# Optimization experiments

Measured on AMD Instinct MI355X. Metric: run time of the kernel, lower is better.

The kernel has to match this reference:

```python
import jax, jax.numpy as jnp
import numpy as np

DISCOUNT_FACTOR = 0.99
AVERAGE_LAMBDA = 0.9
EPS = 1e-8
B, S = 8192, 2048


def setup_inputs() -> dict:
    key = jax.random.key(0)
    k1, k2, k3 = jax.random.split(key, 3)
    values = jax.random.normal(k1, (B, S + 1, 1), jnp.float32)
    rewards = jax.random.normal(k2, (B, S, 1), jnp.float32)
    # binary done flags stored as float, as in the torch module's math
    dones = (jax.random.uniform(k3, (B, S, 1)) < 0.02).astype(jnp.float32)
    # parameter init identical to GammaLambdaLearner.__init__ (atanh of targets)
    raw_gamma = jnp.arctanh(jnp.full((1,), DISCOUNT_FACTOR, jnp.float32))
    raw_lambd = jnp.arctanh(jnp.full((S,), AVERAGE_LAMBDA, jnp.float32))
    return {"values": values, "rewards": rewards, "dones": dones,
            "raw_gamma": raw_gamma, "raw_lambd": raw_lambd}


def reference(values, rewards, dones, raw_gamma, raw_lambd):
    # gamma / lambd properties: tanh then clamp_min(1e-8)
    gamma = jnp.maximum(jnp.tanh(raw_gamma), EPS)          # [1]
    lambd = jnp.maximum(jnp.tanh(raw_lambd), EPS)          # [S]

    # time-major views for the scan: [S, B, 1]
    r = jnp.swapaxes(rewards, 0, 1)
    d = jnp.swapaxes(dones, 0, 1)
    v_next = jnp.swapaxes(values[:, 1:], 0, 1)

    def step(carry, xs):
        # carry: lambda_return[t+1], shape [B, 1]
        r_t, d_t, vn_t, lam_t = xs
        ret = r_t + gamma * (1.0 - d_t) * ((1.0 - lam_t) * vn_t + lam_t * carry)
        return ret, ret

    # backward-in-time recurrence bootstrapped from the final value estimate
    _, outs = jax.lax.scan(step, values[:, -1], (r, d, v_next, lambd), reverse=True)
    return jnp.swapaxes(outs, 0, 1)  # [B, S, 1]
```

## Files before the change

### kernel.cpp

```cpp
#include <hip/hip_runtime.h>
#include <math.h>


#define EPSV 1e-8f

typedef float f32x4 __attribute__((ext_vector_type(4)));

__global__ void precompute_lambda_kernel(const float* __restrict__ raw_gamma,
                                         const float* __restrict__ raw_lambd,
                                         float* __restrict__ lam, int S) {
    int t = blockIdx.x * blockDim.x + threadIdx.x;
    if (t < S) lam[t] = fmaxf(tanhf(raw_lambd[t]), EPSV);
    if (t == S) lam[S] = fmaxf(tanhf(raw_gamma[0]), EPSV);
}

__global__ __launch_bounds__(256) void lamret_kernel(
    const float* __restrict__ values,
    const float* __restrict__ rewards,
    const float* __restrict__ dones,
    const float* __restrict__ raw_gamma,
    const float* __restrict__ raw_lambd,
    const float* __restrict__ lam_pre,
    float* __restrict__ out,
    int S, long vtotal)
{
    constexpr int C = 8;
    __shared__ float aggA[4], aggB[4];

    const int row  = blockIdx.x;
    const int tid  = threadIdx.x;
    const int lane = tid & 63;
    const int wave = tid >> 6;
    const int nwaves = 4;
    const int t0 = tid * C;

    const float* __restrict__ rrow = rewards + (size_t)row * S;
    const float* __restrict__ drow = dones   + (size_t)row * S;
    const float* __restrict__ vrow = values  + (size_t)row * (S + 1);

    const float vlast = vrow[S];

    float gamma;
    if (lam_pre) gamma = lam_pre[S];
    else         gamma = fmaxf(tanhf(raw_gamma[0]), EPSV);

    float a[C], b[C];
    const bool full = (t0 + C <= S) && ((S & 3) == 0);
    if (full) {
        const f32x4* r4 = reinterpret_cast<const f32x4*>(rrow + t0);
        const f32x4* d4 = reinterpret_cast<const f32x4*>(drow + t0);
        f32x4 r01 = r4[0];
        f32x4 r23 = r4[1];
        f32x4 d01 = d4[0];
        f32x4 d23 = d4[1];

        const float* vp = vrow + t0 + 1;
        const int ofs = (int)(((uintptr_t)vp >> 2) & 3);
        const float* base = vp - ofs;
        float vv[C];
        if (ofs == 0) {
            f32x4 w0 = *reinterpret_cast<const f32x4*>(base);
            f32x4 w1 = *reinterpret_cast<const f32x4*>(base + 4);
            #pragma unroll
            for (int i = 0; i < 4; ++i) { vv[i] = w0[i]; vv[4+i] = w1[i]; }
        } else if (base + 12 <= values + vtotal) {
            f32x4 w0 = *reinterpret_cast<const f32x4*>(base);
            f32x4 w1 = *reinterpret_cast<const f32x4*>(base + 4);
            f32x4 w2 = *reinterpret_cast<const f32x4*>(base + 8);
            if (ofs == 1) {
                vv[0]=w0[1]; vv[1]=w0[2]; vv[2]=w0[3];
                vv[3]=w1[0]; vv[4]=w1[1]; vv[5]=w1[2]; vv[6]=w1[3];
                vv[7]=w2[0];
            } else if (ofs == 2) {
                vv[0]=w0[2]; vv[1]=w0[3];
                vv[2]=w1[0]; vv[3]=w1[1]; vv[4]=w1[2]; vv[5]=w1[3];
                vv[6]=w2[0]; vv[7]=w2[1];
            } else {
                vv[0]=w0[3];
                vv[1]=w1[0]; vv[2]=w1[1]; vv[3]=w1[2]; vv[4]=w1[3];
                vv[5]=w2[0]; vv[6]=w2[1]; vv[7]=w2[2];
            }
        } else {
            #pragma unroll
            for (int i = 0; i < C; ++i) vv[i] = vp[i];
        }

        float lm[C];
        if (lam_pre) {
            const f32x4* l4 = reinterpret_cast<const f32x4*>(lam_pre + t0);
            f32x4 l01 = l4[0], l23 = l4[1];
            #pragma unroll
            for (int i = 0; i < 4; ++i) { lm[i] = l01[i]; lm[4+i] = l23[i]; }
        } else {
            #pragma unroll
            for (int i = 0; i < C; ++i) lm[i] = fmaxf(tanhf(raw_lambd[t0 + i]), EPSV);
        }

        float rr[C], dd[C];
        #pragma unroll
        for (int i = 0; i < 4; ++i) { rr[i] = r01[i]; rr[4+i] = r23[i]; }
        #pragma unroll
        for (int i = 0; i < 4; ++i) { dd[i] = d01[i]; dd[4+i] = d23[i]; }

        #pragma unroll
        for (int i = 0; i < C; ++i) {
            float g1d = gamma * (1.0f - dd[i]);
            a[i] = g1d * lm[i];
            b[i] = fmaf(g1d * (1.0f - lm[i]), vv[i], rr[i]);
        }
    } else {
        #pragma unroll
        for (int i = 0; i < C; ++i) {
            int t = t0 + i;
            if (t < S) {
                float lmv = lam_pre ? lam_pre[t] : fmaxf(tanhf(raw_lambd[t]), EPSV);
                float g1d = gamma * (1.0f - drow[t]);
                a[i] = g1d * lmv;
                b[i] = fmaf(g1d * (1.0f - lmv), vrow[t + 1], rrow[t]);
            } else { a[i] = 1.0f; b[i] = 0.0f; }
        }
    }

    float A = 1.0f, Bc = 0.0f;
    #pragma unroll
    for (int i = C - 1; i >= 0; --i) {
        Bc = fmaf(a[i], Bc, b[i]);
        A  = a[i] * A;
    }

    float Ai = A, Bi = Bc;
    #pragma unroll
    for (int off = 1; off < 64; off <<= 1) {
        float Ao = __shfl_down(Ai, off);
        float Bo = __shfl_down(Bi, off);
        if (lane + off < 64) {
            Bi = fmaf(Ai, Bo, Bi);
            Ai = Ai * Ao;
        }
    }
    float Ae = __shfl_down(Ai, 1);
    float Be = __shfl_down(Bi, 1);
    if (lane == 63) { Ae = 1.0f; Be = 0.0f; }

    if (lane == 0) { aggA[wave] = Ai; aggB[wave] = Bi; }
    __syncthreads();
    float TA = 1.0f, TB = 0.0f;
    for (int w2 = wave + 1; w2 < nwaves; ++w2) {
        TB = fmaf(TA, aggB[w2], TB);
        TA = TA * aggA[w2];
    }
    float Af = Ae * TA;
    float Bf = fmaf(Ae, TB, Be);

    float x = fmaf(Af, vlast, Bf);

    float o[C];
    #pragma unroll
    for (int i = C - 1; i >= 0; --i) {
        x = fmaf(a[i], x, b[i]);
        o[i] = x;
    }

    float* __restrict__ orow = out + (size_t)row * S;
    if (full) {
        f32x4* o4 = reinterpret_cast<f32x4*>(orow + t0);
        f32x4 o01, o23;
        #pragma unroll
        for (int i = 0; i < 4; ++i) { o01[i] = o[i]; o23[i] = o[4+i]; }
        __builtin_nontemporal_store(o01, o4);
        __builtin_nontemporal_store(o23, o4 + 1);
    } else {
        for (int i = 0; i < C; ++i)
            if (t0 + i < S) orow[t0 + i] = o[i];
    }
}

extern "C" void kernel_launch(void* const* d_in, const int* in_sizes, int n_in,
                              void* d_out, int out_size, void* d_ws, size_t ws_size,
                              hipStream_t stream) {
    const float* values    = (const float*)d_in[0];
    const float* rewards   = (const float*)d_in[1];
    const float* dones     = (const float*)d_in[2];
    const float* raw_gamma = (const float*)d_in[3];
    const float* raw_lambd = (const float*)d_in[4];
    float* out = (float*)d_out;

    const int S = in_sizes[4];
    const int B = in_sizes[1] / S;
    const long vtotal = in_sizes[0];

    float* lam_pre = nullptr;
    if (ws_size >= (size_t)(S + 1) * sizeof(float)) {
        lam_pre = (float*)d_ws;
        int nthr = 256;
        int nblk = (S + 1 + nthr - 1) / nthr;
        precompute_lambda_kernel<<<nblk, nthr, 0, stream>>>(raw_gamma, raw_lambd, lam_pre, S);
    }

    lamret_kernel<<<B, 256, 0, stream>>>(values, rewards, dones,
                                         raw_gamma, raw_lambd, lam_pre, out, S, vtotal);
}
```

Baseline: 224.0 us.

## Process two rows per block and use nontemporal loads for streamed inputs

```diff
diff --git a/kernel.cpp b/kernel.cpp
--- a/kernel.cpp
+++ b/kernel.cpp
@@ -12,6 +12,100 @@
     int t = blockIdx.x * blockDim.x + threadIdx.x;
     if (t < S) lam[t] = fmaxf(tanhf(raw_lambd[t]), EPSV);
     if (t == S) lam[S] = fmaxf(tanhf(raw_gamma[0]), EPSV);
+}
+
+__device__ __forceinline__ void load_vwindow(const float* __restrict__ vp,
+                                             const float* __restrict__ values,
+                                             long vtotal, float vv[8]) {
+    const int ofs = (int)(((uintptr_t)vp >> 2) & 3);
+    const float* base = vp - ofs;
+    if (ofs == 0) {
+        f32x4 w0 = *reinterpret_cast<const f32x4*>(base);
+        f32x4 w1 = *reinterpret_cast<const f32x4*>(base + 4);
+        #pragma unroll
+        for (int i = 0; i < 4; ++i) { vv[i] = w0[i]; vv[4+i] = w1[i]; }
+    } else if (base + 12 <= values + vtotal) {
+        f32x4 w0 = *reinterpret_cast<const f32x4*>(base);
+        f32x4 w1 = *reinterpret_cast<const f32x4*>(base + 4);
+        f32x4 w2 = *reinterpret_cast<const f32x4*>(base + 8);
+        if (ofs == 1) {
+            vv[0]=w0[1]; vv[1]=w0[2]; vv[2]=w0[3];
+            vv[3]=w1[0]; vv[4]=w1[1]; vv[5]=w1[2]; vv[6]=w1[3];
+            vv[7]=w2[0];
+        } else if (ofs == 2) {
+            vv[0]=w0[2]; vv[1]=w0[3];
+            vv[2]=w1[0]; vv[3]=w1[1]; vv[4]=w1[2]; vv[5]=w1[3];
+            vv[6]=w2[0]; vv[7]=w2[1];
+        } else {
+            vv[0]=w0[3];
+            vv[1]=w1[0]; vv[2]=w1[1]; vv[3]=w1[2]; vv[4]=w1[3];
+            vv[5]=w2[0]; vv[6]=w2[1]; vv[7]=w2[2];
+        }
+    } else {
+        #pragma unroll
+        for (int i = 0; i < 8; ++i) vv[i] = vp[i];
+    }
+}
+
+__device__ __forceinline__ void scan_apply_store(
+    const float a[8], const float b[8], float vlast,
+    float* aggAs, float* aggBs, int lane, int wave,
+    float* __restrict__ orow, int t0, int S, bool full)
+{
+    constexpr int C = 8;
+    const int nwaves = 4;
+
+    float A = 1.0f, Bc = 0.0f;
+    #pragma unroll
+    for (int i = C - 1; i >= 0; --i) {
+        Bc = fmaf(a[i], Bc, b[i]);
+        A  = a[i] * A;
+    }
+
+    float Ai = A, Bi = Bc;
+    #pragma unroll
+    for (int off = 1; off < 64; off <<= 1) {
+        float Ao = __shfl_down(Ai, off);
+        float Bo = __shfl_down(Bi, off);
+        if (lane + off < 64) {
+            Bi = fmaf(Ai, Bo, Bi);
+            Ai = Ai * Ao;
+        }
+    }
+    float Ae = __shfl_down(Ai, 1);
+    float Be = __shfl_down(Bi, 1);
+    if (lane == 63) { Ae = 1.0f; Be = 0.0f; }
+
+    if (lane == 0) { aggAs[wave] = Ai; aggBs[wave] = Bi; }
+    __syncthreads();
+    float TA = 1.0f, TB = 0.0f;
+    for (int w2 = wave + 1; w2 < nwaves; ++w2) {
+        TB = fmaf(TA, aggBs[w2], TB);
+        TA = TA * aggAs[w2];
+    }
+    float Af = Ae * TA;
+    float Bf = fmaf(Ae, TB, Be);
+
+    float x = fmaf(Af, vlast, Bf);
+
+    float o[C];
+    #pragma unroll
+    for (int i = C - 1; i >= 0; --i) {
+        x = fmaf(a[i], x, b[i]);
+        o[i] = x;
+    }
+
+    if (full) {
+        f32x4* o4 = reinterpret_cast<f32x4*>(orow + t0);
+        f32x4 o01, o23;
+        #pragma unroll
+        for (int i = 0; i < 4; ++i) { o01[i] = o[i]; o23[i] = o[4+i]; }
+        __builtin_nontemporal_store(o01, o4);
+        __builtin_nontemporal_store(o23, o4 + 1);
+    } else {
+        for (int i = 0; i < C; ++i)
+            if (t0 + i < S) orow[t0 + i] = o[i];
+    }
 }
 
 __global__ __launch_bounds__(256) void lamret_kernel(
@@ -22,67 +116,60 @@
     const float* __restrict__ raw_lambd,
     const float* __restrict__ lam_pre,
     float* __restrict__ out,
-    int S, long vtotal)
+    int S, long vtotal, int B)
 {
     constexpr int C = 8;
-    __shared__ float aggA[4], aggB[4];
-
-    const int row  = blockIdx.x;
+    __shared__ float aggA[2][4], aggB[2][4];
+
     const int tid  = threadIdx.x;
     const int lane = tid & 63;
     const int wave = tid >> 6;
-    const int nwaves = 4;
-    const int t0 = tid * C;
-
-    const float* __restrict__ rrow = rewards + (size_t)row * S;
-    const float* __restrict__ drow = dones   + (size_t)row * S;
-    const float* __restrict__ vrow = values  + (size_t)row * (S + 1);
-
-    const float vlast = vrow[S];
+    const int t0   = tid * C;
+
+    const int row0 = blockIdx.x * 2;
+    const int row1 = row0 + 1;
+    const bool has1 = (row1 < B);
+
+    const float* __restrict__ rrow0 = rewards + (size_t)row0 * S;
+    const float* __restrict__ drow0 = dones   + (size_t)row0 * S;
+    const float* __restrict__ vrow0 = values  + (size_t)row0 * (S + 1);
+    const float* __restrict__ rrow1 = rewards + (size_t)row1 * S;
+    const float* __restrict__ drow1 = dones   + (size_t)row1 * S;
+    const float* __restrict__ vrow1 = values  + (size_t)row1 * (S + 1);
 
     float gamma;
     if (lam_pre) gamma = lam_pre[S];
     else         gamma = fmaxf(tanhf(raw_gamma[0]), EPSV);
 
-    float a[C], b[C];
+    const float vlast0 = vrow0[S];
+    const float vlast1 = has1 ? vrow1[S] : 0.0f;
+
     const bool full = (t0 + C <= S) && ((S & 3) == 0);
+
+    float a0[C], b0[C], a1[C], b1[C];
     if (full) {
-        const f32x4* r4 = reinterpret_cast<const f32x4*>(rrow + t0);
-        const f32x4* d4 = reinterpret_cast<const f32x4*>(drow + t0);
-        f32x4 r01 = r4[0];
-        f32x4 r23 = r4[1];
-        f32x4 d01 = d4[0];
-        f32x4 d23 = d4[1];
-
-        const float* vp = vrow + t0 + 1;
-        const int ofs = (int)(((uintptr_t)vp >> 2) & 3);
-        const float* base = vp - ofs;
-        float vv[C];
-        if (ofs == 0) {
-            f32x4 w0 = *reinterpret_cast<const f32x4*>(base);
-            f32x4 w1 = *reinterpret_cast<const f32x4*>(base + 4);
-            #pragma unroll
-            for (int i = 0; i < 4; ++i) { vv[i] = w0[i]; vv[4+i] = w1[i]; }
-        } else if (base + 12 <= values + vtotal) {
-            f32x4 w0 = *reinterpret_cast<const f32x4*>(base);
-            f32x4 w1 = *reinterpret_cast<const f32x4*>(base + 4);
-            f32x4 w2 = *reinterpret_cast<const f32x4*>(base + 8);
-            if (ofs == 1) {
-                vv[0]=w0[1]; vv[1]=w0[2]; vv[2]=w0[3];
-                vv[3]=w1[0]; vv[4]=w1[1]; vv[5]=w1[2]; vv[6]=w1[3];
-                vv[7]=w2[0];
-            } else if (ofs == 2) {
-                vv[0]=w0[2]; vv[1]=w0[3];
-                vv[2]=w1[0]; vv[3]=w1[1]; vv[4]=w1[2]; vv[5]=w1[3];
-                vv[6]=w2[0]; vv[7]=w2[1];
-            } else {
-                vv[0]=w0[3];
-                vv[1]=w1[0]; vv[2]=w1[1]; vv[3]=w1[2]; vv[4]=w1[3];
-                vv[5]=w2[0]; vv[6]=w2[1]; vv[7]=w2[2];
-            }
-        } else {
-            #pragma unroll
-            for (int i = 0; i < C; ++i) vv[i] = vp[i];
+        const f32x4* r4_0 = reinterpret_cast<const f32x4*>(rrow0 + t0);
+        const f32x4* d4_0 = reinterpret_cast<const f32x4*>(drow0 + t0);
+        f32x4 r01_0 = __builtin_nontemporal_load(r4_0);
+        f32x4 r23_0 = __builtin_nontemporal_load(r4_0 + 1);
+        f32x4 d01_0 = __builtin_nontemporal_load(d4_0);
+        f32x4 d23_0 = __builtin_nontemporal_load(d4_0 + 1);
+        float vv0[C];
+        load_vwindow(vrow0 + t0 + 1, values, vtotal, vv0);
+
+        f32x4 r01_1 = {0,0,0,0}, r23_1 = {0,0,0,0};
+        f32x4 d01_1 = {0,0,0,0}, d23_1 = {0,0,0,0};
+        float vv1[C];
+        #pragma unroll
+        for (int i = 0; i < C; ++i) vv1[i] = 0.0f;
+        if (has1) {
+            const f32x4* r4_1 = reinterpret_cast<const f32x4*>(rrow1 + t0);
+            const f32x4* d4_1 = reinterpret_cast<const f32x4*>(drow1 + t0);
+            r01_1 = __builtin_nontemporal_load(r4_1);
+            r23_1 = __builtin_nontemporal_load(r4_1 + 1);
+            d01_1 = __builtin_nontemporal_load(d4_1);
+            d23_1 = __builtin_nontemporal_load(d4_1 + 1);
+            load_vwindow(vrow1 + t0 + 1, values, vtotal, vv1);
         }
 
         float lm[C];
@@ -98,15 +185,24 @@
 
         float rr[C], dd[C];
         #pragma unroll
-        for (int i = 0; i < 4; ++i) { rr[i] = r01[i]; rr[4+i] = r23[i]; }
-        #pragma unroll
-        for (int i = 0; i < 4; ++i) { dd[i] = d01[i]; dd[4+i] = d23[i]; }
-
+        for (int i = 0; i < 4; ++i) { rr[i] = r01_0[i]; rr[4+i] = r23_0[i]; }
+        #pragma unroll
+        for (int i = 0; i < 4; ++i) { dd[i] = d01_0[i]; dd[4+i] = d23_0[i]; }
         #pragma unroll
         for (int i = 0; i < C; ++i) {
             float g1d = gamma * (1.0f - dd[i]);
-            a[i] = g1d * lm[i];
-            b[i] = fmaf(g1d * (1.0f - lm[i]), vv[i], rr[i]);
+            a0[i] = g1d * lm[i];
+            b0[i] = fmaf(g1d * (1.0f - lm[i]), vv0[i], rr[i]);
+        }
+        #pragma unroll
+        for (int i = 0; i < 4; ++i) { rr[i] = r01_1[i]; rr[4+i] = r23_1[i]; }
+        #pragma unroll
+        for (int i = 0; i < 4; ++i) { dd[i] = d01_1[i]; dd[4+i] = d23_1[i]; }
+        #pragma unroll
+        for (int i = 0; i < C; ++i) {
+            float g1d = gamma * (1.0f - dd[i]);
+            a1[i] = g1d * lm[i];
+            b1[i] = fmaf(g1d * (1.0f - lm[i]), vv1[i], rr[i]);
         }
     } else {
         #pragma unroll
@@ -114,64 +210,24 @@
             int t = t0 + i;
             if (t < S) {
                 float lmv = lam_pre ? lam_pre[t] : fmaxf(tanhf(raw_lambd[t]), EPSV);
-                float g1d = gamma * (1.0f - drow[t]);
-                a[i] = g1d * lmv;
-                b[i] = fmaf(g1d * (1.0f - lmv), vrow[t + 1], rrow[t]);
-            } else { a[i] = 1.0f; b[i] = 0.0f; }
-        }
-    }
-
-    float A = 1.0f, Bc = 0.0f;
-    #pragma unroll
-    for (int i = C - 1; i >= 0; --i) {
-        Bc = fmaf(a[i], Bc, b[i]);
-        A  = a[i] * A;
-    }
-
-    float Ai = A, Bi = Bc;
-    #pragma unroll
-    for (int off = 1; off < 64; off <<= 1) {
-        float Ao = __shfl_down(Ai, off);
-        float Bo = __shfl_down(Bi, off);
-        if (lane + off < 64) {
-            Bi = fmaf(Ai, Bo, Bi);
-            Ai = Ai * Ao;
-        }
-    }
-    float Ae = __shfl_down(Ai, 1);
-    float Be = __shfl_down(Bi, 1);
-    if (lane == 63) { Ae = 1.0f; Be = 0.0f; }
-
-    if (lane == 0) { aggA[wave] = Ai; aggB[wave] = Bi; }
-    __syncthreads();
-    float TA = 1.0f, TB = 0.0f;
-    for (int w2 = wave + 1; w2 < nwaves; ++w2) {
-        TB = fmaf(TA, aggB[w2], TB);
-        TA = TA * aggA[w2];
-    }
-    float Af = Ae * TA;
-    float Bf = fmaf(Ae, TB, Be);
-
-    float x = fmaf(Af, vlast, Bf);
-
-    float o[C];
-    #pragma unroll
-    for (int i = C - 1; i >= 0; --i) {
-        x = fmaf(a[i], x, b[i]);
-        o[i] = x;
-    }
-
-    float* __restrict__ orow = out + (size_t)row * S;
-    if (full) {
-        f32x4* o4 = reinterpret_cast<f32x4*>(orow + t0);
-        f32x4 o01, o23;
-        #pragma unroll
-        for (int i = 0; i < 4; ++i) { o01[i] = o[i]; o23[i] = o[4+i]; }
-        __builtin_nontemporal_store(o01, o4);
-        __builtin_nontemporal_store(o23, o4 + 1);
-    } else {
-        for (int i = 0; i < C; ++i)
-            if (t0 + i < S) orow[t0 + i] = o[i];
+                float g1d0 = gamma * (1.0f - drow0[t]);
+                a0[i] = g1d0 * lmv;
+                b0[i] = fmaf(g1d0 * (1.0f - lmv), vrow0[t + 1], rrow0[t]);
+                if (has1) {
+                    float g1d1 = gamma * (1.0f - drow1[t]);
+                    a1[i] = g1d1 * lmv;
+                    b1[i] = fmaf(g1d1 * (1.0f - lmv), vrow1[t + 1], rrow1[t]);
+                } else { a1[i] = 1.0f; b1[i] = 0.0f; }
+            } else { a0[i] = 1.0f; b0[i] = 0.0f; a1[i] = 1.0f; b1[i] = 0.0f; }
+        }
+    }
+
+    scan_apply_store(a0, b0, vlast0, aggA[0], aggB[0], lane, wave,
+                     out + (size_t)row0 * S, t0, S, full);
+
+    if (has1) {
+        scan_apply_store(a1, b1, vlast1, aggA[1], aggB[1], lane, wave,
+                         out + (size_t)row1 * S, t0, S, full);
     }
 }
 
@@ -197,6 +253,8 @@
         precompute_lambda_kernel<<<nblk, nthr, 0, stream>>>(raw_gamma, raw_lambd, lam_pre, S);
     }
 
-    lamret_kernel<<<B, 256, 0, stream>>>(values, rewards, dones,
-                                         raw_gamma, raw_lambd, lam_pre, out, S, vtotal);
-}
+    int nblk = (B + 1) / 2;
+    lamret_kernel<<<nblk, 256, 0, stream>>>(values, rewards, dones,
+                                            raw_gamma, raw_lambd, lam_pre, out,
+                                            S, vtotal, B);
+}
```

After: 212.6 us. -5.1%, faster.

## Split each row into two coalesced halves with interleaved block scans for S=2048

Applied to the files above, without the earlier changes.

```diff
diff --git a/kernel.cpp b/kernel.cpp
--- a/kernel.cpp
+++ b/kernel.cpp
@@ -12,6 +12,58 @@
     int t = blockIdx.x * blockDim.x + threadIdx.x;
     if (t < S) lam[t] = fmaxf(tanhf(raw_lambd[t]), EPSV);
     if (t == S) lam[S] = fmaxf(tanhf(raw_gamma[0]), EPSV);
+}
+
+__device__ __forceinline__ void load_v4(const float* __restrict__ vp,
+                                        const float* __restrict__ lo,
+                                        const float* __restrict__ hi,
+                                        float vv[4]) {
+    const int s = (int)(((uintptr_t)vp >> 2) & 3);
+    const float* base = vp - s;
+    if (s == 0) {
+        f32x4 w0 = *reinterpret_cast<const f32x4*>(base);
+        vv[0] = w0[0]; vv[1] = w0[1]; vv[2] = w0[2]; vv[3] = w0[3];
+    } else if (base >= lo && base + 8 <= hi) {
+        f32x4 w0 = *reinterpret_cast<const f32x4*>(base);
+        f32x4 w1 = *reinterpret_cast<const f32x4*>(base + 4);
+        if (s == 1)      { vv[0]=w0[1]; vv[1]=w0[2]; vv[2]=w0[3]; vv[3]=w1[0]; }
+        else if (s == 2) { vv[0]=w0[2]; vv[1]=w0[3]; vv[2]=w1[0]; vv[3]=w1[1]; }
+        else             { vv[0]=w0[3]; vv[1]=w1[0]; vv[2]=w1[1]; vv[3]=w1[2]; }
+    } else {
+        vv[0] = vp[0]; vv[1] = vp[1]; vv[2] = vp[2]; vv[3] = vp[3];
+    }
+}
+
+__device__ __forceinline__ void block_suffix_scan(
+    float A, float Bc, float* aggAs, float* aggBs, int lane, int wave,
+    float& Af, float& Bf, float& GA, float& GB)
+{
+    float Ai = A, Bi = Bc;
+    #pragma unroll
+    for (int off = 1; off < 64; off <<= 1) {
+        float Ao = __shfl_down(Ai, off);
+        float Bo = __shfl_down(Bi, off);
+        if (lane + off < 64) { Bi = fmaf(Ai, Bo, Bi); Ai = Ai * Ao; }
+    }
+    float Ae = __shfl_down(Ai, 1);
+    float Be = __shfl_down(Bi, 1);
+    if (lane == 63) { Ae = 1.0f; Be = 0.0f; }
+
+    if (lane == 0) { aggAs[wave] = Ai; aggBs[wave] = Bi; }
+    __syncthreads();
+    float TA = 1.0f, TB = 0.0f;
+    for (int w2 = wave + 1; w2 < 4; ++w2) {
+        TB = fmaf(TA, aggBs[w2], TB);
+        TA = TA * aggAs[w2];
+    }
+    Af = Ae * TA;
+    Bf = fmaf(Ae, TB, Be);
+    GA = 1.0f; GB = 0.0f;
+    #pragma unroll
+    for (int w2 = 0; w2 < 4; ++w2) {
+        GB = fmaf(GA, aggBs[w2], GB);
+        GA = GA * aggAs[w2];
+    }
 }
 
 __global__ __launch_bounds__(256) void lamret_kernel(
@@ -24,91 +76,95 @@
     float* __restrict__ out,
     int S, long vtotal)
 {
-    constexpr int C = 8;
-    __shared__ float aggA[4], aggB[4];
+    __shared__ float aggA[2][4], aggB[2][4];
 
     const int row  = blockIdx.x;
     const int tid  = threadIdx.x;
     const int lane = tid & 63;
     const int wave = tid >> 6;
-    const int nwaves = 4;
-    const int t0 = tid * C;
 
     const float* __restrict__ rrow = rewards + (size_t)row * S;
     const float* __restrict__ drow = dones   + (size_t)row * S;
     const float* __restrict__ vrow = values  + (size_t)row * (S + 1);
-
-    const float vlast = vrow[S];
+    float* __restrict__ orow = out + (size_t)row * S;
 
     float gamma;
     if (lam_pre) gamma = lam_pre[S];
     else         gamma = fmaxf(tanhf(raw_gamma[0]), EPSV);
 
-    float a[C], b[C];
-    const bool full = (t0 + C <= S) && ((S & 3) == 0);
-    if (full) {
-        const f32x4* r4 = reinterpret_cast<const f32x4*>(rrow + t0);
-        const f32x4* d4 = reinterpret_cast<const f32x4*>(drow + t0);
-        f32x4 r01 = r4[0];
-        f32x4 r23 = r4[1];
-        f32x4 d01 = d4[0];
-        f32x4 d23 = d4[1];
-
-        const float* vp = vrow + t0 + 1;
-        const int ofs = (int)(((uintptr_t)vp >> 2) & 3);
-        const float* base = vp - ofs;
-        float vv[C];
-        if (ofs == 0) {
-            f32x4 w0 = *reinterpret_cast<const f32x4*>(base);
-            f32x4 w1 = *reinterpret_cast<const f32x4*>(base + 4);
+    const float vlast = vrow[S];
+
+    if (S == 2048) {
+        constexpr int C = 4;
+        const int HALF = 1024;
+        const int t1 = tid * C;
+        const int t2 = HALF + tid * C;
+
+        f32x4 r1 = __builtin_nontemporal_load(reinterpret_cast<const f32x4*>(rrow + t1));
+        f32x4 r2 = __builtin_nontemporal_load(reinterpret_cast<const f32x4*>(rrow + t2));
+        f32x4 d1 = __builtin_nontemporal_load(reinterpret_cast<const f32x4*>(drow + t1));
+        f32x4 d2 = __builtin_nontemporal_load(reinterpret_cast<const f32x4*>(drow + t2));
+
+        float vv1[C], vv2[C];
+        load_v4(vrow + t1 + 1, values, values + vtotal, vv1);
+        load_v4(vrow + t2 + 1, values, values + vtotal, vv2);
+
+        float lm1[C], lm2[C];
+        if (lam_pre) {
+            f32x4 l1 = *reinterpret_cast<const f32x4*>(lam_pre + t1);
+            f32x4 l2 = *reinterpret_cast<const f32x4*>(lam_pre + t2);
             #pragma unroll
-            for (int i = 0; i < 4; ++i) { vv[i] = w0[i]; vv[4+i] = w1[i]; }
-        } else if (base + 12 <= values + vtotal) {
-            f32x4 w0 = *reinterpret_cast<const f32x4*>(base);
-            f32x4 w1 = *reinterpret_cast<const f32x4*>(base + 4);
-            f32x4 w2 = *reinterpret_cast<const f32x4*>(base + 8);
-            if (ofs == 1) {
-                vv[0]=w0[1]; vv[1]=w0[2]; vv[2]=w0[3];
-                vv[3]=w1[0]; vv[4]=w1[1]; vv[5]=w1[2]; vv[6]=w1[3];
-                vv[7]=w2[0];
-            } else if (ofs == 2) {
-                vv[0]=w0[2]; vv[1]=w0[3];
-                vv[2]=w1[0]; vv[3]=w1[1]; vv[4]=w1[2]; vv[5]=w1[3];
-                vv[6]=w2[0]; vv[7]=w2[1];
-            } else {
-                vv[0]=w0[3];
-                vv[1]=w1[0]; vv[2]=w1[1]; vv[3]=w1[2]; vv[4]=w1[3];
-                vv[5]=w2[0]; vv[6]=w2[1]; vv[7]=w2[2];
-            }
+            for (int i = 0; i < C; ++i) { lm1[i] = l1[i]; lm2[i] = l2[i]; }
         } else {
             #pragma unroll
-            for (int i = 0; i < C; ++i) vv[i] = vp[i];
-        }
-
-        float lm[C];
-        if (lam_pre) {
-            const f32x4* l4 = reinterpret_cast<const f32x4*>(lam_pre + t0);
-            f32x4 l01 = l4[0], l23 = l4[1];
-            #pragma unroll
-            for (int i = 0; i < 4; ++i) { lm[i] = l01[i]; lm[4+i] = l23[i]; }
-        } else {
-            #pragma unroll
-            for (int i = 0; i < C; ++i) lm[i] = fmaxf(tanhf(raw_lambd[t0 + i]), EPSV);
-        }
-
-        float rr[C], dd[C];
-        #pragma unroll
-        for (int i = 0; i < 4; ++i) { rr[i] = r01[i]; rr[4+i] = r23[i]; }
-        #pragma unroll
-        for (int i = 0; i < 4; ++i) { dd[i] = d01[i]; dd[4+i] = d23[i]; }
-
+            for (int i = 0; i < C; ++i) {
+                lm1[i] = fmaxf(tanhf(raw_lambd[t1 + i]), EPSV);
+                lm2[i] = fmaxf(tanhf(raw_lambd[t2 + i]), EPSV);
+            }
+        }
+
+        float a1[C], b1[C], a2[C], b2[C];
         #pragma unroll
         for (int i = 0; i < C; ++i) {
-            float g1d = gamma * (1.0f - dd[i]);
-            a[i] = g1d * lm[i];
-            b[i] = fmaf(g1d * (1.0f - lm[i]), vv[i], rr[i]);
-        }
+            float g1d = gamma * (1.0f - d1[i]);
+            a1[i] = g1d * lm1[i];
+            b1[i] = fmaf(g1d * (1.0f - lm1[i]), vv1[i], r1[i]);
+        }
+        #pragma unroll
+        for (int i = 0; i < C; ++i) {
+            float g1d = gamma * (1.0f - d2[i]);
+            a2[i] = g1d * lm2[i];
+            b2[i] = fmaf(g1d * (1.0f - lm2[i]), vv2[i], r2[i]);
+        }
+
+        float A1 = 1.0f, B1 = 0.0f, A2 = 1.0f, B2 = 0.0f;
+        #pragma unroll
+        for (int i = C - 1; i >= 0; --i) {
+            B1 = fmaf(a1[i], B1, b1[i]);  A1 = a1[i] * A1;
+            B2 = fmaf(a2[i], B2, b2[i]);  A2 = a2[i] * A2;
+        }
+
+        float Af2, Bf2, G2A, G2B;
+        block_suffix_scan(A2, B2, aggA[1], aggB[1], lane, wave, Af2, Bf2, G2A, G2B);
+        float x2 = fmaf(Af2, vlast, Bf2);
+
+        float Af1, Bf1, G1A, G1B;
+        block_suffix_scan(A1, B1, aggA[0], aggB[0], lane, wave, Af1, Bf1, G1A, G1B);
+        float xg = fmaf(G2A, vlast, G2B);
+        float x1 = fmaf(Af1, xg, Bf1);
+
+        f32x4 o1, o2;
+        #pragma unroll
+        for (int i = C - 1; i >= 0; --i) {
+            x2 = fmaf(a2[i], x2, b2[i]);  o2[i] = x2;
+            x1 = fmaf(a1[i], x1, b1[i]);  o1[i] = x1;
+        }
+        __builtin_nontemporal_store(o1, reinterpret_cast<f32x4*>(orow + t1));
+        __builtin_nontemporal_store(o2, reinterpret_cast<f32x4*>(orow + t2));
     } else {
+        constexpr int C = 8;
+        const int t0 = tid * C;
+        float a[C], b[C];
         #pragma unroll
         for (int i = 0; i < C; ++i) {
             int t = t0 + i;
@@ -119,59 +175,20 @@
                 b[i] = fmaf(g1d * (1.0f - lmv), vrow[t + 1], rrow[t]);
             } else { a[i] = 1.0f; b[i] = 0.0f; }
         }
-    }
-
-    float A = 1.0f, Bc = 0.0f;
-    #pragma unroll
-    for (int i = C - 1; i >= 0; --i) {
-        Bc = fmaf(a[i], Bc, b[i]);
-        A  = a[i] * A;
-    }
-
-    float Ai = A, Bi = Bc;
-    #pragma unroll
-    for (int off = 1; off < 64; off <<= 1) {
-        float Ao = __shfl_down(Ai, off);
-        float Bo = __shfl_down(Bi, off);
-        if (lane + off < 64) {
-            Bi = fmaf(Ai, Bo, Bi);
-            Ai = Ai * Ao;
-        }
-    }
-    float Ae = __shfl_down(Ai, 1);
-    float Be = __shfl_down(Bi, 1);
-    if (lane == 63) { Ae = 1.0f; Be = 0.0f; }
-
-    if (lane == 0) { aggA[wave] = Ai; aggB[wave] = Bi; }
-    __syncthreads();
-    float TA = 1.0f, TB = 0.0f;
-    for (int w2 = wave + 1; w2 < nwaves; ++w2) {
-        TB = fmaf(TA, aggB[w2], TB);
-        TA = TA * aggA[w2];
-    }
-    float Af = Ae * TA;
-    float Bf = fmaf(Ae, TB, Be);
-
-    float x = fmaf(Af, vlast, Bf);
-
-    float o[C];
-    #pragma unroll
-    for (int i = C - 1; i >= 0; --i) {
-        x = fmaf(a[i], x, b[i]);
-        o[i] = x;
-    }
-
-    float* __restrict__ orow = out + (size_t)row * S;
-    if (full) {
-        f32x4* o4 = reinterpret_cast<f32x4*>(orow + t0);
-        f32x4 o01, o23;
-        #pragma unroll
-        for (int i = 0; i < 4; ++i) { o01[i] = o[i]; o23[i] = o[4+i]; }
-        __builtin_nontemporal_store(o01, o4);
-        __builtin_nontemporal_store(o23, o4 + 1);
-    } else {
-        for (int i = 0; i < C; ++i)
-            if (t0 + i < S) orow[t0 + i] = o[i];
+        float A = 1.0f, Bc = 0.0f;
+        #pragma unroll
+        for (int i = C - 1; i >= 0; --i) {
+            Bc = fmaf(a[i], Bc, b[i]);
+            A  = a[i] * A;
+        }
+        float Af, Bf, GA, GB;
+        block_suffix_scan(A, Bc, aggA[0], aggB[0], lane, wave, Af, Bf, GA, GB);
+        float x = fmaf(Af, vlast, Bf);
+        #pragma unroll
+        for (int i = C - 1; i >= 0; --i) {
+            x = fmaf(a[i], x, b[i]);
+            if (t0 + i < S) orow[t0 + i] = x;
+        }
     }
 }
 
```

After: 206.0 us. -8.0%, faster.
